# Performance work log

Measured on AMD Instinct MI355X. Metric: run time of the kernel, lower is better.

The kernel has to match this reference:

```python
import jax, jax.numpy as jnp
import numpy as np

E, K, CAP = 6, 2, 192
ALPHA, LOAD_PEN, MIN_USE, TEMP = 0.7, 2.0, 0.05, 1.0
BN_EPS = 1e-5
NEG = -1e30


def conv3x3(x, w, b=None):
    y = jax.lax.conv_general_dilated(x, w, (1, 1), 'SAME',
                                     dimension_numbers=('NCHW', 'OIHW', 'NCHW'))
    if b is not None:
        y = y + b[None, :, None, None]
    return y


def bn_eval(x, g, b):
    # fresh BatchNorm buffers: running_mean=0, running_var=1
    s = g / jnp.sqrt(1.0 + BN_EPS)
    return x * s[None, :, None, None] + b[None, :, None, None]


def maxpool2(x):
    return jax.lax.reduce_window(x, -jnp.inf, jax.lax.max,
                                 (1, 1, 2, 2), (1, 1, 2, 2), 'VALID')


def avgpool_to2(x):
    B, C, H, W = x.shape
    return x.reshape(B, C, 2, H // 2, 2, W // 2).mean(axis=(3, 5))


def expert_forward(p, x):
    h = jax.nn.relu(bn_eval(conv3x3(x, p['c1w'], p['c1b']), p['b1g'], p['b1b']))
    h = maxpool2(h)  # 32 -> 16
    h = jax.nn.relu(bn_eval(conv3x3(h, p['c2w'], p['c2b']), p['b2g'], p['b2b']))
    h = jax.nn.relu(bn_eval(conv3x3(h, p['c3w'], p['c3b']), p['b3g'], p['b3b']))
    h = maxpool2(h)  # 16 -> 8
    h = jax.nn.relu(bn_eval(conv3x3(h, p['c4w'], p['c4b']), p['b4g'], p['b4b']))
    h = jax.nn.relu(bn_eval(conv3x3(h, p['c5w'], p['c5b']), p['b5g'], p['b5b']))
    feat = h.mean(axis=(2, 3))                       # global avg pool -> [B, c3]
    f = jax.nn.relu(feat @ p['fw'].T + p['fb'])      # [B, feat_dim]
    return f @ p['cw'].T + p['cb']                   # [B, num_classes]


def moe_forward(x, t_c1w, t_b1g, t_b1b, t_c2w, t_b2g, t_b2b, t_fcw, t_fcb,
                g1w, g1b, g2w, g2b,
                e_c1w, e_c1b, e_b1g, e_b1b, e_c2w, e_c2b, e_b2g, e_b2b,
                e_c3w, e_c3b, e_b3g, e_b3b, e_c4w, e_c4b, e_b4g, e_b4b,
                e_c5w, e_c5b, e_b5g, e_b5b, e_fw, e_fb, e_cw, e_cb, ema):
    B = x.shape[0]
    # --- routing trunk ---
    h = jax.nn.relu(bn_eval(conv3x3(x, t_c1w), t_b1g, t_b1b))
    h = jax.nn.relu(bn_eval(conv3x3(h, t_c2w), t_b2g, t_b2b))
    h = avgpool_to2(maxpool2(h)).reshape(B, -1)      # [B, 128]
    rf = jax.nn.relu(h @ t_fcw.T + t_fcb)            # [B, routing_dim]
    # --- gate (eval: no dropout, no noise) ---
    g = jax.nn.relu(rf @ g1w.T + g1b)
    gate_scores = (g @ g2w.T + g2b) / TEMP           # [B, E]
    # --- all experts on full batch (dense, as in source) ---
    ep = {'c1w': e_c1w, 'c1b': e_c1b, 'b1g': e_b1g, 'b1b': e_b1b,
          'c2w': e_c2w, 'c2b': e_c2b, 'b2g': e_b2g, 'b2b': e_b2b,
          'c3w': e_c3w, 'c3b': e_c3b, 'b3g': e_b3g, 'b3b': e_b3b,
          'c4w': e_c4w, 'c4b': e_c4b, 'b4g': e_b4g, 'b4b': e_b4b,
          'c5w': e_c5w, 'c5b': e_c5b, 'b5g': e_b5g, 'b5b': e_b5b,
          'fw': e_fw, 'fb': e_fb, 'cw': e_cw, 'cb': e_cb}
    logits_e = jax.vmap(expert_forward, in_axes=(0, None))(ep, x)  # [E, B, C]
    logits_e = jnp.transpose(logits_e, (1, 0, 2))                   # [B, E, C]
    # confidence = -entropy = sum p*log(p)
    logp = jax.nn.log_softmax(logits_e, axis=2)
    conf = (jnp.exp(logp) * jnp.log(jnp.exp(logp) + 1e-12)).sum(axis=2)  # [B, E]
    # --- balanced scores ---
    combined = ALPHA * gate_scores + (1.0 - ALPHA) * conf
    boost = jnp.where(ema < MIN_USE, (MIN_USE - ema) * 10.0, 0.0)
    combined = combined + boost[None, :]
    balanced = combined - LOAD_PEN * ema[None, :]
    # --- greedy capacity-constrained dispatch (deterministic order, eval) ---
    _, topk_idx = jax.lax.top_k(balanced, K)          # [B, K]

    def step(loads, idxs):
        l = loads[idxs]                                # [K]
        fits = l < CAP
        first = jnp.argmax(fits)                       # first expert with room
        fallback = idxs[jnp.argmin(l)]
        chosen = jnp.where(fits.any(), idxs[first], fallback)
        return loads.at[chosen].add(1.0), chosen

    _, chosen = jax.lax.scan(step, jnp.zeros((E,), balanced.dtype), topk_idx)
    D = jax.nn.one_hot(chosen, E, dtype=bool)          # [B, E]
    # --- weighted combine ---
    masked = jnp.where(D, balanced, NEG)
    w = jax.nn.softmax(masked, axis=1) * D.astype(balanced.dtype)
    w = w / (w.sum(axis=1, keepdims=True) + 1e-12)
    logits_final = (w[:, :, None] * logits_e).sum(axis=1)  # [B, C]
    return logits_final, balanced, D


def _params(key):
    ks = iter(jax.random.split(key, 64))
    rd, rd2, fd, nc, c1, c2, c3 = 64, 32, 128, 10, 32, 64, 128

    def w(shape, fan):
        return jax.random.normal(next(ks), shape, jnp.float32) * np.sqrt(2.0 / fan)

    p = {}
    p['t_c1w'] = w((32, 3, 3, 3), 32 * 9); p['t_b1g'] = jnp.ones(32); p['t_b1b'] = jnp.zeros(32)
    p['t_c2w'] = w((32, 32, 3, 3), 32 * 9); p['t_b2g'] = jnp.ones(32); p['t_b2b'] = jnp.zeros(32)
    p['t_fcw'] = w((rd, 128), rd); p['t_fcb'] = jnp.zeros(rd)
    p['g1w'] = w((rd2, rd), rd2); p['g1b'] = jnp.zeros(rd2)
    p['g2w'] = w((E, rd2), E); p['g2b'] = jnp.zeros(E)
    for i, (ci, co) in enumerate([(3, c1), (c1, c2), (c2, c2), (c2, c3), (c3, c3)], 1):
        p[f'e_c{i}w'] = w((E, co, ci, 3, 3), co * 9)
        p[f'e_c{i}b'] = jnp.zeros((E, co))
        p[f'e_b{i}g'] = jnp.ones((E, co))
        p[f'e_b{i}b'] = jnp.zeros((E, co))
    p['e_fw'] = w((E, fd, c3), fd); p['e_fb'] = jnp.zeros((E, fd))
    p['e_cw'] = w((E, nc, fd), nc); p['e_cb'] = jnp.zeros((E, nc))
    p['ema'] = jnp.ones((E,), jnp.float32) / E
    return p


def setup_inputs() -> dict:
    key = jax.random.key(0)
    kx, kp = jax.random.split(key)
    inp = {'x': jax.random.normal(kx, (1024, 3, 32, 32), jnp.float32)}
    inp.update(_params(kp))
    return inp


def reference(x, t_c1w, t_b1g, t_b1b, t_c2w, t_b2g, t_b2b, t_fcw, t_fcb,
              g1w, g1b, g2w, g2b,
              e_c1w, e_c1b, e_b1g, e_b1b, e_c2w, e_c2b, e_b2g, e_b2b,
              e_c3w, e_c3b, e_b3g, e_b3b, e_c4w, e_c4b, e_b4g, e_b4b,
              e_c5w, e_c5b, e_b5g, e_b5b, e_fw, e_fb, e_cw, e_cb, ema):
    return moe_forward(x, t_c1w, t_b1g, t_b1b, t_c2w, t_b2g, t_b2b, t_fcw, t_fcb,
                       g1w, g1b, g2w, g2b,
                       e_c1w, e_c1b, e_b1g, e_b1b, e_c2w, e_c2b, e_b2g, e_b2b,
                       e_c3w, e_c3b, e_b3g, e_b3b, e_c4w, e_c4b, e_b4g, e_b4b,
                       e_c5w, e_c5b, e_b5g, e_b5b, e_fw, e_fb, e_cw, e_cb, ema)
```

## Files before the change

kernel.cpp:

```cpp
#include <hip/hip_runtime.h>
#include <math.h>

#define B_ 1024
#define E_ 6

typedef _Float16 half8 __attribute__((ext_vector_type(8)));
typedef float f32x4 __attribute__((ext_vector_type(4)));

__device__ __forceinline__ unsigned short h_bits(_Float16 h) {
    union { _Float16 f; unsigned short u; } c; c.f = h; return c.u;
}
__device__ __forceinline__ unsigned int splitpack(float v) {
    _Float16 h = (_Float16)v;
    _Float16 l = (_Float16)((v - (float)h) * 2048.0f);
    return (unsigned int)h_bits(h) | ((unsigned int)h_bits(l) << 16);
}

__global__ void prep_w(const float* __restrict__ w, const float* __restrict__ g,
                       float* __restrict__ wout, int CO, int CI, int total) {
    int i = blockIdx.x * 256 + threadIdx.x;
    if (i >= total) return;
    int k = i % 9;
    int t = i / 9;
    int ci = t % CI; t /= CI;
// ... 154 lines not shown
                }
                *(uint4*)(po + base + cobase + j4) = u;
            }
        }
    } else {
        float* out = (float*)outv;
        if constexpr (POOL) {
            constexpr int HP = H / 2;
            int py = ty / 2 + oy;
            int pxx = tx / 2 + ox;
#pragma unroll
            for (int g2 = 0; g2 < GPT; ++g2)
#pragma unroll
                for (int j = 0; j < CO_BLK; ++j) {
                    int co = (cg0s + g2 * G) * CO_BLK + j;
                    int a = g2 * CO_BLK + j;
                    float m = fmaxf(fmaxf(acc[0][a], acc[1][a]), fmaxf(acc[2][a], acc[3][a]));
                    out[((long)n * CO + co) * (HP * HP) + py * HP + pxx] = fmaxf(m, 0.0f);
                }
        } else {
            int yy = ty + oy;
            int xx = tx + ox;
#pragma unroll
            for (int g2 = 0; g2 < GPT; ++g2)
#pragma unroll
                for (int j = 0; j < CO_BLK; ++j) {
                    int co = (cg0s + g2 * G) * CO_BLK + j;
                    out[((long)n * CO + co) * (H * H) + yy * H + xx] =
                        fmaxf(acc[0][g2 * CO_BLK + j], 0.0f);
                }
        }
    }
}

__launch_bounds__(256, 2)
__global__ void conv_mfma_t2(const unsigned int* __restrict__ in,
                             const _Float16* __restrict__ wt,
                             const float* __restrict__ bias,
                             float* __restrict__ rf, int n0) {
    constexpr int PXS = 40;
    __shared__ _Float16 ldsH[18 * 18 * PXS];
    __shared__ _Float16 ldsL[18 * 18 * PXS];
    __shared__ float red[4][32];

    const int tid = threadIdx.x;
    const int wv = tid >> 6, lane = tid & 63;
    const int q = lane >> 4, l15 = lane & 15;
    const int bid = blockIdx.x;
    const int nl = bid >> 2, tile = bid & 3;
    const int ty2 = (tile >> 1) * 16, tx2 = (tile & 1) * 16;

    f32x4 accH[8], accL[8];
#pragma unroll
    for (int i = 0; i < 8; ++i) { accH[i] = (f32x4){0,0,0,0}; accL[i] = (f32x4){0,0,0,0}; }

    for (int u = tid; u < 18 * 18 * 8; u += 256) {
        int cu = u & 7;
        int p = u >> 3;
        int wy = p / 18, wx = p % 18;
        int gy = ty2 + wy - 1, gx = tx2 + wx - 1;
        uint4 w = make_uint4(0, 0, 0, 0);
        if ((unsigned)gy < 32u && (unsigned)gx < 32u)
            w = *(const uint4*)(in + ((long)nl * 1024 + gy * 32 + gx) * 32 + cu * 4);
        unsigned int h01 = (w.x & 0xffffu) | (w.y << 16);
        unsigned int h23 = (w.z & 0xffffu) | (w.w << 16);
        unsigned int l01 = (w.x >> 16) | (w.y & 0xffff0000u);
        unsigned int l23 = (w.z >> 16) | (w.w & 0xffff0000u);
        int fi = (wy * 18 + wx) * PXS + cu * 4;
        *(uint2*)(&ldsH[fi]) = make_uint2(h01, h23);
        *(uint2*)(&ldsL[fi]) = make_uint2(l01, l23);
    }
    __syncthreads();

#pragma unroll
    for (int ky = 0; ky < 3; ++ky)
#pragma unroll
        for (int kx = 0; kx < 3; ++kx) {
            const int tap = ky * 3 + kx;
            half8 ah[4], al[4];
#pragma unroll
            for (int mb = 0; mb < 4; ++mb) {
                int y = wv * 4 + mb;
                int fi = ((y + ky) * 18 + (l15 + kx)) * PXS + q * 8;
                ah[mb] = *(const half8*)&ldsH[fi];
                al[mb] = *(const half8*)&ldsL[fi];
            }
            half8 bh[2], bl[2];
#pragma unroll
            for (int nb = 0; nb < 2; ++nb) {
                int F0 = (nb * 9 + tap) * 2;
                bh[nb] = ((const half8*)wt)[(long)F0 * 64 + lane];
                bl[nb] = ((const half8*)wt)[(long)(F0 + 1) * 64 + lane];
            }
#pragma unroll
            for (int nb = 0; nb < 2; ++nb)
#pragma unroll
                for (int mb = 0; mb < 4; ++mb)
                    accH[mb * 2 + nb] = __builtin_amdgcn_mfma_f32_16x16x32_f16(
                        ah[mb], bh[nb], accH[mb * 2 + nb], 0, 0, 0);
#pragma unroll
            for (int nb = 0; nb < 2; ++nb)
#pragma unroll
                for (int mb = 0; mb < 4; ++mb)
                    accL[mb * 2 + nb] = __builtin_amdgcn_mfma_f32_16x16x32_f16(
                        ah[mb], bl[nb], accL[mb * 2 + nb], 0, 0, 0);
#pragma unroll
            for (int nb = 0; nb < 2; ++nb)
#pragma unroll
                for (int mb = 0; mb < 4; ++mb)
                    accL[mb * 2 + nb] = __builtin_amdgcn_mfma_f32_16x16x32_f16(
                        al[mb], bh[nb], accL[mb * 2 + nb], 0, 0, 0);
        }

    const float inv2048 = 1.0f / 2048.0f;
    float bv[2];
#pragma unroll
    for (int nb = 0; nb < 2; ++nb) bv[nb] = bias[nb * 16 + l15];
    float avg[2] = {0.0f, 0.0f};
#pragma unroll
    for (int k = 0; k < 2; ++k)
#pragma unroll
        for (int j = 0; j < 2; ++j)
#pragma unroll
            for (int nb = 0; nb < 2; ++nb) {
                float m = -1e30f;
#pragma unroll
                for (int dm = 0; dm < 2; ++dm)
#pragma unroll
                    for (int dr = 0; dr < 2; ++dr) {
                        int a = (2 * k + dm) * 2 + nb;
                        int r = 2 * j + dr;
                        float v = accH[a][r] + accL[a][r] * inv2048 + bv[nb];
                        m = fmaxf(m, v);
                    }
                avg[nb] += fmaxf(m, 0.0f);
            }
#pragma unroll
    for (int nb = 0; nb < 2; ++nb) {
        avg[nb] += __shfl_xor(avg[nb], 16);
        avg[nb] += __shfl_xor(avg[nb], 32);
    }
    if (q == 0) {
        red[wv][l15] = avg[0];
        red[wv][16 + l15] = avg[1];
    }
    __syncthreads();
    if (tid < 32) {
        float s = red[0][tid] + red[1][tid] + red[2][tid] + red[3][tid];
        int n = n0 + nl;
        rf[(long)n * 128 + tid * 4 + (tile >> 1) * 2 + (tile & 1)] = s * (1.0f / 64.0f);
    }
}

__launch_bounds__(512, 2)
__global__ void conv_expert(const float* __restrict__ x,
                            const float* __restrict__ w1b, const float* __restrict__ b1b_,
                            const _Float16* __restrict__ wt2b, const float* __restrict__ b2b_,
                            const _Float16* __restrict__ wt3b, const float* __restrict__ b3b_,
                            const _Float16* __restrict__ wt4b, const float* __restrict__ b4b_,
                            const _Float16* __restrict__ wt5b, const float* __restrict__ b5b_,
                            float* __restrict__ featb) {
    __shared__ _Float16 pool[77760];
    _Float16* c2H = pool;
    _Float16* c2L = pool + 12960;
    _Float16* BH  = pool;
    _Float16* BL  = pool + 8000;
    float* xs  = (float*)(pool + 25920);
    float* w1s = (float*)(pool + 25920 + 6936);
    float* b1s = (float*)(pool + 25920 + 6936 + 1728);
    _Float16* AH = pool + 25920;
    _Float16* AL = pool + 51840;
    _Float16* CH = pool + 25920;
    _Float16* CL = pool + 41920;

    const int tid = threadIdx.x;
    const int wv = tid >> 6, lane = tid & 63;
    const int q = lane >> 4, l15 = lane & 15;
    const int rg = wv >> 1, ch2 = wv & 1;
    const int e = blockIdx.x >> 10;
    const int n = blockIdx.x & 1023;
    const float inv2048 = 1.0f / 2048.0f;

    const float* w1 = w1b + e * 864;
    const float* b1 = b1b_ + e * 32;
    const _Float16* wt2 = wt2b + (size_t)e * 36864;
    const float* b2 = b2b_ + e * 64;
    const _Float16* wt3 = wt3b + (size_t)e * 73728;
    const float* b3 = b3b_ + e * 64;
    const _Float16* wt4 = wt4b + (size_t)e * 147456;
    const float* b4 = b4b_ + e * 128;
    const _Float16* wt5 = wt5b + (size_t)e * 294912;
    const float* b5 = b5b_ + e * 128;
    float* feat = featb + (size_t)e * (B_ * 128);

    {
        half8 z = {};
        half8* zp = (half8*)pool;
        for (int i = tid; i < 3240; i += 512) zp[i] = z;
    }
    for (int i = tid; i < 864; i += 512) w1s[i] = w1[i];
    if (tid < 32) b1s[tid] = b1[tid];
    for (int i = tid; i < 3 * 1156; i += 512) {
        int c = i / 1156;
        int r = i - c * 1156;
        int yy = r / 34 - 1, xx = r % 34 - 1;
        float v = 0.0f;
        if ((unsigned)yy < 32u && (unsigned)xx < 32u)
            v = x[((long)n * 3 + c) * 1024 + yy * 32 + xx];
        xs[i] = v;
    }
    __syncthreads();

    {
        const int pix = tid & 255;
        const int py1 = pix >> 4, px1 = pix & 15;
        const int coh = tid >> 8;
#pragma unroll
        for (int cg = 0; cg < 2; ++cg) {
            const int cog = coh * 2 + cg;
            float a[4][8];
#pragma unroll
            for (int j = 0; j < 8; ++j) {
                float bvv = b1s[cog * 8 + j];
#pragma unroll
                for (int p = 0; p < 4; ++p) a[p][j] = bvv;
            }
            for (int ci = 0; ci < 3; ++ci) {
                float patch[16];
#pragma unroll
                for (int r = 0; r < 4; ++r)
#pragma unroll
                    for (int cpx = 0; cpx < 4; ++cpx)
                        patch[r * 4 + cpx] = xs[ci * 1156 + (2 * py1 + r) * 34 + (2 * px1 + cpx)];
#pragma unroll
                for (int ky = 0; ky < 3; ++ky)
#pragma unroll
                    for (int kx = 0; kx < 3; ++kx) {
                        const float* wr = &w1s[((ci * 3 + ky) * 3 + kx) * 32 + cog * 8];
#pragma unroll
                        for (int j = 0; j < 8; ++j) {
                            float wvv = wr[j];
#pragma unroll
                            for (int dy = 0; dy < 2; ++dy)
#pragma unroll
                                for (int dx = 0; dx < 2; ++dx)
                                    a[dy * 2 + dx][j] =
                                        fmaf(patch[(dy + ky) * 4 + (dx + kx)], wvv,
                                             a[dy * 2 + dx][j]);
                        }
                    }
            }
            int fibase = ((py1 + 1) * 18 + (px1 + 1)) * 40 + cog * 8;
#pragma unroll
            for (int j = 0; j < 8; ++j) {
                float m = fmaxf(fmaxf(a[0][j], a[1][j]), fmaxf(a[2][j], a[3][j]));
                m = fmaxf(m, 0.0f);
                _Float16 hi = (_Float16)m;
                _Float16 lo = (_Float16)((m - (float)hi) * 2048.0f);
                c2H[fibase + j] = hi;
                c2L[fibase + j] = lo;
            }
        }
    }
    __syncthreads();

    for (int u = tid; u < 2 * 68 * 5; u += 512) {
        int g = u % 5;
        int t2 = u / 5;
        int ck = t2 / 68;
        int rp = t2 % 68;
        int wy, wx;
        if (rp < 18) { wy = 0; wx = rp; }
        else if (rp < 36) { wy = 17; wx = rp - 18; }
        else if (rp < 52) { wy = rp - 35; wx = 0; }
        else { wy = rp - 51; wx = 17; }
        int fi = ck * 12960 + (wy * 18 + wx) * 40 + g * 8;
        *(uint4*)(&AH[fi]) = make_uint4(0, 0, 0, 0);
        *(uint4*)(&AL[fi]) = make_uint4(0, 0, 0, 0);
    }

    f32x4 accH[8], accL[8];
#pragma unroll
    for (int i = 0; i < 8; ++i) { accH[i] = (f32x4){0,0,0,0}; accL[i] = (f32x4){0,0,0,0}; }

#pragma unroll
    for (int ky = 0; ky < 3; ++ky)
#pragma unroll
        for (int kx = 0; kx < 3; ++kx) {
            const int tap = ky * 3 + kx;
            half8 ah[4], al[4];
#pragma unroll
            for (int mb = 0; mb < 4; ++mb) {
                int y = rg * 4 + mb;
                int fi = ((y + ky) * 18 + (l15 + kx)) * 40 + q * 8;
                ah[mb] = *(const half8*)&c2H[fi];
                al[mb] = *(const half8*)&c2L[fi];
            }
            half8 bh[2], bl[2];
#pragma unroll
            for (int nb = 0; nb < 2; ++nb) {
                int nbg = ch2 * 2 + nb;
                int F0 = (nbg * 9 + tap) * 2;
                bh[nb] = ((const half8*)wt2)[(long)F0 * 64 + lane];
                bl[nb] = ((const half8*)wt2)[(long)(F0 + 1) * 64 + lane];
            }
#pragma unroll
            for (int nb = 0; nb < 2; ++nb)
#pragma unroll
                for (int mb = 0; mb < 4; ++mb)
                    accH[mb * 2 + nb] = __builtin_amdgcn_mfma_f32_16x16x32_f16(
                        ah[mb], bh[nb], accH[mb * 2 + nb], 0, 0, 0);
#pragma unroll
            for (int nb = 0; nb < 2; ++nb)
#pragma unroll
                for (int mb = 0; mb < 4; ++mb)
                    accL[mb * 2 + nb] = __builtin_amdgcn_mfma_f32_16x16x32_f16(
                        ah[mb], bl[nb], accL[mb * 2 + nb], 0, 0, 0);
#pragma unroll
            for (int nb = 0; nb < 2; ++nb)
#pragma unroll
                for (int mb = 0; mb < 4; ++mb)
                    accL[mb * 2 + nb] = __builtin_amdgcn_mfma_f32_16x16x32_f16(
                        al[mb], bh[nb], accL[mb * 2 + nb], 0, 0, 0);
        }
    {
        float bv[2];
#pragma unroll
        for (int nb = 0; nb < 2; ++nb) bv[nb] = b2[ch2 * 32 + nb * 16 + l15];
#pragma unroll
        for (int mb = 0; mb < 4; ++mb) {
            int y = rg * 4 + mb;
#pragma unroll
            for (int r = 0; r < 4; ++r) {
                int p = (y + 1) * 18 + (q * 4 + r + 1);
#pragma unroll
                for (int nb = 0; nb < 2; ++nb) {
                    float v = accH[mb * 2 + nb][r] + accL[mb * 2 + nb][r] * inv2048 + bv[nb];
                    v = fmaxf(v, 0.0f);
                    _Float16 hi = (_Float16)v;
                    _Float16 lo = (_Float16)((v - (float)hi) * 2048.0f);
                    int fi = ch2 * 12960 + p * 40 + nb * 16 + l15;
                    AH[fi] = hi;
                    AL[fi] = lo;
                }
            }
        }
    }
    __syncthreads();

#pragma unroll
    for (int i = 0; i < 8; ++i) { accH[i] = (f32x4){0,0,0,0}; accL[i] = (f32x4){0,0,0,0}; }

    for (int c = 0; c < 2; ++c) {
#pragma unroll
        for (int ky = 0; ky < 3; ++ky)
#pragma unroll
            for (int kx = 0; kx < 3; ++kx) {
                const int tap = ky * 3 + kx;
                half8 ah[4], al[4];
#pragma unroll
                for (int mb = 0; mb < 4; ++mb) {
                    int y = rg * 4 + mb;
                    int fi = c * 12960 + ((y + ky) * 18 + (l15 + kx)) * 40 + q * 8;
                    ah[mb] = *(const half8*)&AH[fi];
                    al[mb] = *(const half8*)&AL[fi];
                }
                half8 bh[2], bl[2];
#pragma unroll
                for (int nb = 0; nb < 2; ++nb) {
                    int nbg = ch2 * 2 + nb;
                    int F0 = ((nbg * 9 + tap) * 2 + c) * 2;
                    bh[nb] = ((const half8*)wt3)[(long)F0 * 64 + lane];
                    bl[nb] = ((const half8*)wt3)[(long)(F0 + 1) * 64 + lane];
                }
#pragma unroll
                for (int nb = 0; nb < 2; ++nb)
#pragma unroll
                    for (int mb = 0; mb < 4; ++mb)
                        accH[mb * 2 + nb] = __builtin_amdgcn_mfma_f32_16x16x32_f16(
                            ah[mb], bh[nb], accH[mb * 2 + nb], 0, 0, 0);
#pragma unroll
                for (int nb = 0; nb < 2; ++nb)
#pragma unroll
                    for (int mb = 0; mb < 4; ++mb)
                        accL[mb * 2 + nb] = __builtin_amdgcn_mfma_f32_16x16x32_f16(
                            ah[mb], bl[nb], accL[mb * 2 + nb], 0, 0, 0);
#pragma unroll
                for (int nb = 0; nb < 2; ++nb)
#pragma unroll
                    for (int mb = 0; mb < 4; ++mb)
                        accL[mb * 2 + nb] = __builtin_amdgcn_mfma_f32_16x16x32_f16(
                            al[mb], bh[nb], accL[mb * 2 + nb], 0, 0, 0);
            }
    }
    __syncthreads();

    for (int u = tid; u < 2 * 36 * 4; u += 512) {
        int g = u & 3;
        int t2 = u >> 2;
        int ck = t2 / 36;
        int rp = t2 % 36;
        int wy, wx;
        if (rp < 10) { wy = 0; wx = rp; }
        else if (rp < 20) { wy = 9; wx = rp - 10; }
        else if (rp < 28) { wy = rp - 19; wx = 0; }
        else { wy = rp - 27; wx = 9; }
        int fi = ck * 4000 + (wy * 10 + wx) * 40 + g * 8;
        *(uint4*)(&BH[fi]) = make_uint4(0, 0, 0, 0);
        *(uint4*)(&BL[fi]) = make_uint4(0, 0, 0, 0);
    }
    for (int u = tid; u < 4 * 36 * 4; u += 512) {
        int g = u & 3;
        int t2 = u >> 2;
        int ck = t2 / 36;
        int rp = t2 % 36;
        int wy, wx;
        if (rp < 10) { wy = 0; wx = rp; }
        else if (rp < 20) { wy = 9; wx = rp - 10; }
        else if (rp < 28) { wy = rp - 19; wx = 0; }
        else { wy = rp - 27; wx = 9; }
        int fi = ck * 4000 + (wy * 10 + wx) * 40 + g * 8;
        *(uint4*)(&CH[fi]) = make_uint4(0, 0, 0, 0);
        *(uint4*)(&CL[fi]) = make_uint4(0, 0, 0, 0);
    }
    {
        float bv[2];
#pragma unroll
        for (int nb = 0; nb < 2; ++nb) bv[nb] = b3[ch2 * 32 + nb * 16 + l15];
#pragma unroll
        for (int k = 0; k < 2; ++k)
#pragma unroll
            for (int j = 0; j < 2; ++j) {
                int yy = rg * 2 + k;
                int xx = q * 2 + j;
                int p = (yy + 1) * 10 + (xx + 1);
#pragma unroll
                for (int nb = 0; nb < 2; ++nb) {
                    float m = -1e30f;
#pragma unroll
                    for (int dm = 0; dm < 2; ++dm)
#pragma unroll
                        for (int dr = 0; dr < 2; ++dr) {
                            int a = (2 * k + dm) * 2 + nb;
                            int r = 2 * j + dr;
                            float v = accH[a][r] + accL[a][r] * inv2048 + bv[nb];
                            m = fmaxf(m, v);
                        }
                    m = fmaxf(m, 0.0f);
                    _Float16 hi = (_Float16)m;
                    _Float16 lo = (_Float16)((m - (float)hi) * 2048.0f);
                    int fi = ch2 * 4000 + p * 40 + nb * 16 + l15;
                    BH[fi] = hi;
                    BL[fi] = lo;
                }
            }
    }
    __syncthreads();

#pragma unroll
    for (int i = 0; i < 4; ++i) { accH[i] = (f32x4){0,0,0,0}; accL[i] = (f32x4){0,0,0,0}; }

    for (int c = 0; c < 2; ++c) {
#pragma unroll
        for (int ky = 0; ky < 3; ++ky)
#pragma unroll
            for (int kx = 0; kx < 3; ++kx) {
                const int tap = ky * 3 + kx;
                half8 ah[4], al[4];
#pragma unroll
                for (int mb = 0; mb < 4; ++mb) {
                    int m = mb * 16 + l15;
                    int p = ((m >> 3) + ky) * 10 + ((m & 7) + kx);
                    int fi = c * 4000 + p * 40 + q * 8;
                    ah[mb] = *(const half8*)&BH[fi];
                    al[mb] = *(const half8*)&BL[fi];
                }
                half8 bh, bl;
                {
                    int F0 = ((wv * 9 + tap) * 2 + c) * 2;
                    bh = ((const half8*)wt4)[(long)F0 * 64 + lane];
                    bl = ((const half8*)wt4)[(long)(F0 + 1) * 64 + lane];
                }
#pragma unroll
                for (int mb = 0; mb < 4; ++mb)
                    accH[mb] = __builtin_amdgcn_mfma_f32_16x16x32_f16(ah[mb], bh, accH[mb], 0, 0, 0);
#pragma unroll
                for (int mb = 0; mb < 4; ++mb)
                    accL[mb] = __builtin_amdgcn_mfma_f32_16x16x32_f16(ah[mb], bl, accL[mb], 0, 0, 0);
#pragma unroll
                for (int mb = 0; mb < 4; ++mb)
                    accL[mb] = __builtin_amdgcn_mfma_f32_16x16x32_f16(al[mb], bh, accL[mb], 0, 0, 0);
            }
    }
    {
        float bv = b4[wv * 16 + l15];
#pragma unroll
        for (int mb = 0; mb < 4; ++mb)
#pragma unroll
            for (int r = 0; r < 4; ++r) {
                int px = mb * 16 + q * 4 + r;
                int p = ((px >> 3) + 1) * 10 + ((px & 7) + 1);
                float v = accH[mb][r] + accL[mb][r] * inv2048 + bv;
                v = fmaxf(v, 0.0f);
                _Float16 hi = (_Float16)v;
                _Float16 lo = (_Float16)((v - (float)hi) * 2048.0f);
                int fi = (wv >> 1) * 4000 + p * 40 + (wv & 1) * 16 + l15;
                CH[fi] = hi;
                CL[fi] = lo;
            }
    }
    __syncthreads();

#pragma unroll
    for (int i = 0; i < 4; ++i) { accH[i] = (f32x4){0,0,0,0}; accL[i] = (f32x4){0,0,0,0}; }

    for (int c = 0; c < 4; ++c) {
#pragma unroll
        for (int ky = 0; ky < 3; ++ky)
#pragma unroll
            for (int kx = 0; kx < 3; ++kx) {
                const int tap = ky * 3 + kx;
                half8 ah[4], al[4];
#pragma unroll
                for (int mb = 0; mb < 4; ++mb) {
                    int m = mb * 16 + l15;
                    int p = ((m >> 3) + ky) * 10 + ((m & 7) + kx);
                    int fi = c * 4000 + p * 40 + q * 8;
                    ah[mb] = *(const half8*)&CH[fi];
                    al[mb] = *(const half8*)&CL[fi];
                }
                half8 bh, bl;
                {
                    int F0 = ((wv * 9 + tap) * 4 + c) * 2;
                    bh = ((const half8*)wt5)[(long)F0 * 64 + lane];
                    bl = ((const half8*)wt5)[(long)(F0 + 1) * 64 + lane];
                }
#pragma unroll
                for (int mb = 0; mb < 4; ++mb)
                    accH[mb] = __builtin_amdgcn_mfma_f32_16x16x32_f16(ah[mb], bh, accH[mb], 0, 0, 0);
#pragma unroll
                for (int mb = 0; mb < 4; ++mb)
                    accL[mb] = __builtin_amdgcn_mfma_f32_16x16x32_f16(ah[mb], bl, accL[mb], 0, 0, 0);
#pragma unroll
                for (int mb = 0; mb < 4; ++mb)
                    accL[mb] = __builtin_amdgcn_mfma_f32_16x16x32_f16(al[mb], bh, accL[mb], 0, 0, 0);
            }
    }
    {
        float bv = b5[wv * 16 + l15];
        float s = 0.0f;
#pragma unroll
        for (int mb = 0; mb < 4; ++mb)
#pragma unroll
            for (int r = 0; r < 4; ++r) {
                float v = accH[mb][r] + accL[mb][r] * inv2048 + bv;
                s += fmaxf(v, 0.0f);
            }
        s += __shfl_xor(s, 16);
        s += __shfl_xor(s, 32);
        if (lane < 16)
            feat[(long)n * 128 + wv * 16 + l15] = s * (1.0f / 64.0f);
    }
}

__launch_bounds__(128)
__global__ void head_k(const float* __restrict__ featb, const float* __restrict__ fwb,
                       const float* __restrict__ fbb, const float* __restrict__ cwb,
                       const float* __restrict__ cbb, float* __restrict__ outlb) {
    __shared__ float fe[128];
    __shared__ float fv[128];
    int e = blockIdx.x >> 10;
    int n = blockIdx.x & 1023;
    int t = threadIdx.x;
    const float* feat = featb + (size_t)e * (B_ * 128);
    const float* fw = fwb + (size_t)e * 16384;
    const float* fb = fbb + e * 128;
    const float* cw = cwb + (size_t)e * 1280;
    const float* cb = cbb + e * 10;
    float* outl = outlb + (size_t)e * (B_ * 10);

    fe[t] = feat[(long)n * 128 + t];
    __syncthreads();
    const float* wr = fw + t * 128;
    float a = fb[t];
#pragma unroll 8
    for (int k = 0; k < 128; ++k) a = fmaf(fe[k], wr[k], a);
    fv[t] = fmaxf(a, 0.0f);
    __syncthreads();
    if (t < 10) {
        const float* cr = cw + t * 128;
        float a2 = cb[t];
#pragma unroll 8
        for (int k = 0; k < 128; ++k) a2 = fmaf(fv[k], cr[k], a2);
        outl[n * 10 + t] = a2;
    }
}

template <int I, int O, bool RELU>
__global__ void fc_k(const float* __restrict__ in, const float* __restrict__ W,
                     const float* __restrict__ bias, float* __restrict__ out) {
    int g = blockIdx.x * 256 + threadIdx.x;
    if (g >= B_ * O) return;
    int n = g / O;
    int o = g - n * O;
    const float* ip = in + (long)n * I;
    const float* wp = W + (long)o * I;
    float a = bias[o];
#pragma unroll 8
    for (int k = 0; k < I; ++k) a = fmaf(ip[k], wp[k], a);
    if (RELU) a = fmaxf(a, 0.0f);
    out[g] = a;
}

__global__ void conf_bal_k(const float* __restrict__ logitsE, const float* __restrict__ gate,
                           const float* __restrict__ ema, float* __restrict__ balanced,
                           unsigned char* __restrict__ cand) {
    int b = blockIdx.x * 256 + threadIdx.x;
    if (b >= B_) return;
    float bal[E_];
#pragma unroll
    for (int e = 0; e < E_; ++e) {
        const float* lp = logitsE + ((long)e * B_ + b) * 10;
        float m = lp[0];
#pragma unroll
        for (int k = 1; k < 10; ++k) m = fmaxf(m, lp[k]);
        float s = 0.0f;
#pragma unroll
        for (int k = 0; k < 10; ++k) s += expf(lp[k] - m);
        float ls = m + logf(s);
        float conf = 0.0f;
#pragma unroll
        for (int k = 0; k < 10; ++k) {
            float pp = expf(lp[k] - ls);
            conf += pp * logf(pp + 1e-12f);
        }
        float em = ema[e];
        float boost = (em < 0.05f) ? (0.05f - em) * 10.0f : 0.0f;
        bal[e] = 0.7f * gate[b * E_ + e] + 0.3f * conf + boost - 2.0f * em;
        balanced[b * E_ + e] = bal[e];
    }
    int i0 = 0;
    float m0 = bal[0];
#pragma unroll
    for (int e = 1; e < E_; ++e)
        if (bal[e] > m0) { m0 = bal[e]; i0 = e; }
    int i1 = -1;
    float m1 = -1e38f;
#pragma unroll
    for (int e = 0; e < E_; ++e)
        if (e != i0 && bal[e] > m1) { m1 = bal[e]; i1 = e; }
    cand[b] = (unsigned char)(i0 | (i1 << 3));
}

__global__ void dispatch_k(const unsigned char* __restrict__ cand, int* __restrict__ chosen) {
    int lane = threadIdx.x;
    unsigned long long L = 0;
    for (int r = 0; r < 16; ++r) {
        unsigned int v = cand[r * 64 + lane];
        int ch = 0;
        for (int q2 = 0; q2 < 64; ++q2) {
            unsigned int s = (unsigned int)__builtin_amdgcn_readlane((int)v, q2);
            unsigned int i0 = s & 7u;
            unsigned int i1 = (s >> 3) & 7u;
            unsigned int a0 = (unsigned int)(L >> (i0 * 10)) & 1023u;
            unsigned int a1 = (unsigned int)(L >> (i1 * 10)) & 1023u;
            unsigned int fb = (a1 < a0) ? i1 : i0;
            unsigned int c = (a0 < 192u) ? i0 : ((a1 < 192u) ? i1 : fb);
            if (lane == q2) ch = (int)c;
            L += 1ull << (c * 10);
        }
        chosen[r * 64 + lane] = ch;
    }
}

__global__ void final_k(const float* __restrict__ logitsE, const int* __restrict__ chosen,
                        float* __restrict__ out) {
    int b = blockIdx.x * 256 + threadIdx.x;
    if (b >= B_) return;
    int c = chosen[b];
    const float w = 1.0f / (1.0f + 1e-12f);
    const float* lp = logitsE + ((long)c * B_ + b) * 10;
#pragma unroll
    for (int k = 0; k < 10; ++k) out[b * 10 + k] = lp[k] * w;
    float* Dp = out + B_ * 10 + B_ * E_ + b * E_;
#pragma unroll
    for (int e = 0; e < E_; ++e) Dp[e] = (e == c) ? 1.0f : 0.0f;
}

extern "C" void kernel_launch(void* const* d_in, const int* in_sizes, int n_in,
                              void* d_out, int out_size, void* d_ws, size_t ws_size,
                              hipStream_t stream) {
    (void)in_sizes; (void)n_in; (void)out_size; (void)ws_size;
    const float* x     = (const float*)d_in[0];
    const float* t_c1w = (const float*)d_in[1];
    const float* t_b1g = (const float*)d_in[2];
    const float* t_b1b = (const float*)d_in[3];
    const float* t_c2w = (const float*)d_in[4];
    const float* t_b2g = (const float*)d_in[5];
    const float* t_b2b = (const float*)d_in[6];
    const float* t_fcw = (const float*)d_in[7];
    const float* t_fcb = (const float*)d_in[8];
    const float* g1w   = (const float*)d_in[9];
    const float* g1b   = (const float*)d_in[10];
    const float* g2w   = (const float*)d_in[11];
    const float* g2b   = (const float*)d_in[12];
    const float* e_c1w = (const float*)d_in[13];
    const float* e_c1b = (const float*)d_in[14];
    const float* e_b1g = (const float*)d_in[15];
    const float* e_b1b = (const float*)d_in[16];
    const float* e_c2w = (const float*)d_in[17];
    const float* e_c2b = (const float*)d_in[18];
    const float* e_b2g = (const float*)d_in[19];
    const float* e_b2b = (const float*)d_in[20];
    const float* e_c3w = (const float*)d_in[21];
    const float* e_c3b = (const float*)d_in[22];
    const float* e_b3g = (const float*)d_in[23];
    const float* e_b3b = (const float*)d_in[24];
    const float* e_c4w = (const float*)d_in[25];
    const float* e_c4b = (const float*)d_in[26];
    const float* e_b4g = (const float*)d_in[27];
    const float* e_b4b = (const float*)d_in[28];
    const float* e_c5w = (const float*)d_in[29];
    const float* e_c5b = (const float*)d_in[30];
    const float* e_b5g = (const float*)d_in[31];
    const float* e_b5b = (const float*)d_in[32];
    const float* e_fw  = (const float*)d_in[33];
    const float* e_fb  = (const float*)d_in[34];
    const float* e_cw  = (const float*)d_in[35];
    const float* e_cb  = (const float*)d_in[36];
    const float* ema   = (const float*)d_in[37];
    float* out = (float*)d_out;
    float* ws  = (float*)d_ws;

    size_t o = 0;
    float* R1f = ws + o; o += 8388608;
    float* R2f = ws + o; o += 16777216;
    float* rf_in   = ws + o; o += B_ * 128;
    float* rf      = ws + o; o += B_ * 64;
    float* gv      = ws + o; o += B_ * 32;
    float* gate    = ws + o; o += B_ * E_;
    float* logitsE = ws + o; o += E_ * B_ * 10;
    float* featb   = ws + o; o += (size_t)E_ * B_ * 128;
    int*   chosen  = (int*)(ws + o); o += B_;
    unsigned char* cand = (unsigned char*)(ws + o); o += 256;
    float* wt_t1 = ws + o; o += 864;
    float* bt_t1 = ws + o; o += 32;
    float* bt_t2 = ws + o; o += 32;
    float* wt_c1 = ws + o; o += 6 * 864;
    float* bt_c1 = ws + o; o += 6 * 32;
    float* bt_c2 = ws + o; o += 6 * 64;
    float* bt_c3 = ws + o; o += 6 * 64;
    float* bt_c4 = ws + o; o += 6 * 128;
    float* bt_c5 = ws + o; o += 6 * 128;
    _Float16* wfrag_t2 = (_Float16*)(ws + o); o += 9216;
    _Float16* wfrag_c2 = (_Float16*)(ws + o); o += 110592;
    _Float16* wfrag_c3 = (_Float16*)(ws + o); o += 221184;
    _Float16* wfrag_c4 = (_Float16*)(ws + o); o += 442368;
    _Float16* wfrag_c5 = (_Float16*)(ws + o); o += 884736;

    unsigned int* R2u = (unsigned int*)R2f;
    (void)R1f;

    auto gsz = [](int n) { return (n + 255) / 256; };
    prep_w<<<gsz(864), 256, 0, stream>>>(t_c1w, t_b1g, wt_t1, 32, 3, 864);
    prep_b<<<1, 256, 0, stream>>>(nullptr, t_b1g, t_b1b, bt_t1, 32);
    prep_wfrag<<<gsz(9216), 256, 0, stream>>>(t_c2w, t_b2g, wfrag_t2, 32, 32, 9216);
    prep_b<<<1, 256, 0, stream>>>(nullptr, t_b2g, t_b2b, bt_t2, 32);
    prep_w<<<gsz(5184), 256, 0, stream>>>(e_c1w, e_b1g, wt_c1, 32, 3, 5184);
    prep_b<<<1, 256, 0, stream>>>(e_c1b, e_b1g, e_b1b, bt_c1, 192);
    prep_wfrag<<<gsz(110592), 256, 0, stream>>>(e_c2w, e_b2g, wfrag_c2, 32, 64, 110592);
    prep_b<<<2, 256, 0, stream>>>(e_c2b, e_b2g, e_b2b, bt_c2, 384);
    prep_wfrag<<<gsz(221184), 256, 0, stream>>>(e_c3w, e_b3g, wfrag_c3, 64, 64, 221184);
    prep_b<<<2, 256, 0, stream>>>(e_c3b, e_b3g, e_b3b, bt_c3, 384);
    prep_wfrag<<<gsz(442368), 256, 0, stream>>>(e_c4w, e_b4g, wfrag_c4, 64, 128, 442368);
    prep_b<<<3, 256, 0, stream>>>(e_c4b, e_b4g, e_b4b, bt_c4, 768);
    prep_wfrag<<<gsz(884736), 256, 0, stream>>>(e_c5w, e_b5g, wfrag_c5, 128, 128, 884736);
    prep_b<<<3, 256, 0, stream>>>(e_c5b, e_b5g, e_b5b, bt_c5, 768);

    for (int q = 0; q < 2; ++q) {
        const float* xq = x + (size_t)q * 512 * 3 * 1024;
        conv3x3<3, 32, 32, 16, 32, 3, false, 1><<<512 * 4, 256, 0, stream>>>(
            xq, wt_t1, bt_t1, (void*)R2u);
        conv_mfma_t2<<<512 * 4, 256, 0, stream>>>(R2u, wfrag_t2, bt_t2, rf_in, q * 512);
    }
    fc_k<128, 64, true><<<256, 256, 0, stream>>>(rf_in, t_fcw, t_fcb, rf);
    fc_k<64, 32, true><<<128, 256, 0, stream>>>(rf, g1w, g1b, gv);
    fc_k<32, 6, false><<<24, 256, 0, stream>>>(gv, g2w, g2b, gate);

    conv_expert<<<E_ * B_, 512, 0, stream>>>(
        x, wt_c1, bt_c1, wfrag_c2, bt_c2, wfrag_c3, bt_c3,
        wfrag_c4, bt_c4, wfrag_c5, bt_c5, featb);
    head_k<<<E_ * B_, 128, 0, stream>>>(featb, e_fw, e_fb, e_cw, e_cb, logitsE);

    float* balanced = out + B_ * 10;
    conf_bal_k<<<4, 256, 0, stream>>>(logitsE, gate, ema, balanced, cand);
    dispatch_k<<<1, 64, 0, stream>>>(cand, chosen);
    final_k<<<4, 256, 0, stream>>>(logitsE, chosen, out);
}
```

Before: 1.325 ms.

## Double conv_expert block to 1024 threads, splitting MFMA tiles across 16 waves

Expands the fused per-image expert conv kernel from 8 to 16 waves. Each wave now handles half the output rows or pixels in every conv stage, with smaller accumulator and fragment arrays. Conv4/5 add a pixel-half split and a shared-memory reduction for the global average pool. The aim is more latency hiding per block, since LDS use (~155KB) already limits occupancy to one block per CU. The cost is duplicated weight-fragment loads per wave and an extra barrier.

```diff
diff --git a/kernel.cpp b/kernel.cpp
--- a/kernel.cpp
+++ b/kernel.cpp
@@ -330,7 +330,7 @@
     }
 }
 
-__launch_bounds__(512, 2)
+__launch_bounds__(1024, 1)
 __global__ void conv_expert(const float* __restrict__ x,
                             const float* __restrict__ w1b, const float* __restrict__ b1b_,
                             const _Float16* __restrict__ wt2b, const float* __restrict__ b2b_,
@@ -354,7 +354,8 @@
     const int tid = threadIdx.x;
     const int wv = tid >> 6, lane = tid & 63;
     const int q = lane >> 4, l15 = lane & 15;
-    const int rg = wv >> 1, ch2 = wv & 1;
+    const int rg3 = wv >> 1, ch2 = wv & 1;
+    const int nbg45 = wv >> 1, ph45 = wv & 1;
     const int e = blockIdx.x >> 10;
     const int n = blockIdx.x & 1023;
     const float inv2048 = 1.0f / 2048.0f;
@@ -374,11 +375,11 @@
     {
         half8 z = {};
         half8* zp = (half8*)pool;
-        for (int i = tid; i < 3240; i += 512) zp[i] = z;
-    }
-    for (int i = tid; i < 864; i += 512) w1s[i] = w1[i];
-    if (tid < 32) b1s[tid] = b1[tid];
-    for (int i = tid; i < 3 * 1156; i += 512) {
+        for (int i = tid; i < 3240; i += 1024) zp[i] = z;
+    }
+    if (tid < 864) w1s[tid] = w1[tid];
+    if (tid >= 896 && tid < 928) b1s[tid - 896] = b1[tid - 896];
+    for (int i = tid; i < 3 * 1156; i += 1024) {
         int c = i / 1156;
         int r = i - c * 1156;
         int yy = r / 34 - 1, xx = r % 34 - 1;
@@ -392,57 +393,53 @@
     {
         const int pix = tid & 255;
         const int py1 = pix >> 4, px1 = pix & 15;
-        const int coh = tid >> 8;
-#pragma unroll
-        for (int cg = 0; cg < 2; ++cg) {
-            const int cog = coh * 2 + cg;
-            float a[4][8];
-#pragma unroll
-            for (int j = 0; j < 8; ++j) {
-                float bvv = b1s[cog * 8 + j];
-#pragma unroll
-                for (int p = 0; p < 4; ++p) a[p][j] = bvv;
-            }
-            for (int ci = 0; ci < 3; ++ci) {
-                float patch[16];
-#pragma unroll
-                for (int r = 0; r < 4; ++r)
-#pragma unroll
-                    for (int cpx = 0; cpx < 4; ++cpx)
-                        patch[r * 4 + cpx] = xs[ci * 1156 + (2 * py1 + r) * 34 + (2 * px1 + cpx)];
-#pragma unroll
-                for (int ky = 0; ky < 3; ++ky)
-#pragma unroll
-                    for (int kx = 0; kx < 3; ++kx) {
-                        const float* wr = &w1s[((ci * 3 + ky) * 3 + kx) * 32 + cog * 8];
-#pragma unroll
-                        for (int j = 0; j < 8; ++j) {
-                            float wvv = wr[j];
-#pragma unroll
-                            for (int dy = 0; dy < 2; ++dy)
-#pragma unroll
-                                for (int dx = 0; dx < 2; ++dx)
-                                    a[dy * 2 + dx][j] =
-                                        fmaf(patch[(dy + ky) * 4 + (dx + kx)], wvv,
-                                             a[dy * 2 + dx][j]);
-                        }
+        const int cog = tid >> 8;
+        float a[4][8];
+#pragma unroll
+        for (int j = 0; j < 8; ++j) {
+            float bvv = b1s[cog * 8 + j];
+#pragma unroll
+            for (int p = 0; p < 4; ++p) a[p][j] = bvv;
+        }
+        for (int ci = 0; ci < 3; ++ci) {
+            float patch[16];
+#pragma unroll
+            for (int r = 0; r < 4; ++r)
+#pragma unroll
+                for (int cpx = 0; cpx < 4; ++cpx)
+                    patch[r * 4 + cpx] = xs[ci * 1156 + (2 * py1 + r) * 34 + (2 * px1 + cpx)];
+#pragma unroll
+            for (int ky = 0; ky < 3; ++ky)
+#pragma unroll
+                for (int kx = 0; kx < 3; ++kx) {
+                    const float* wr = &w1s[((ci * 3 + ky) * 3 + kx) * 32 + cog * 8];
+#pragma unroll
+                    for (int j = 0; j < 8; ++j) {
+                        float wvv = wr[j];
+#pragma unroll
+                        for (int dy = 0; dy < 2; ++dy)
+#pragma unroll
+                            for (int dx = 0; dx < 2; ++dx)
+                                a[dy * 2 + dx][j] =
+                                    fmaf(patch[(dy + ky) * 4 + (dx + kx)], wvv,
+                                         a[dy * 2 + dx][j]);
                     }
-            }
-            int fibase = ((py1 + 1) * 18 + (px1 + 1)) * 40 + cog * 8;
-#pragma unroll
-            for (int j = 0; j < 8; ++j) {
-                float m = fmaxf(fmaxf(a[0][j], a[1][j]), fmaxf(a[2][j], a[3][j]));
-                m = fmaxf(m, 0.0f);
-                _Float16 hi = (_Float16)m;
-                _Float16 lo = (_Float16)((m - (float)hi) * 2048.0f);
-                c2H[fibase + j] = hi;
-                c2L[fibase + j] = lo;
-            }
+                }
+        }
+        int fibase = ((py1 + 1) * 18 + (px1 + 1)) * 40 + cog * 8;
+#pragma unroll
+        for (int j = 0; j < 8; ++j) {
+            float m = fmaxf(fmaxf(a[0][j], a[1][j]), fmaxf(a[2][j], a[3][j]));
+            m = fmaxf(m, 0.0f);
+            _Float16 hi = (_Float16)m;
+            _Float16 lo = (_Float16)((m - (float)hi) * 2048.0f);
+            c2H[fibase + j] = hi;
+            c2L[fibase + j] = lo;
         }
     }
     __syncthreads();
 
-    for (int u = tid; u < 2 * 68 * 5; u += 512) {
+    for (int u = tid; u < 2 * 68 * 5; u += 1024) {
         int g = u % 5;
         int t2 = u / 5;
         int ck = t2 / 68;
@@ -457,19 +454,19 @@
         *(uint4*)(&AL[fi]) = make_uint4(0, 0, 0, 0);
     }
 
-    f32x4 accH[8], accL[8];
-#pragma unroll
-    for (int i = 0; i < 8; ++i) { accH[i] = (f32x4){0,0,0,0}; accL[i] = (f32x4){0,0,0,0}; }
+    f32x4 accH[4], accL[4];
+#pragma unroll
+    for (int i = 0; i < 4; ++i) { accH[i] = (f32x4){0,0,0,0}; accL[i] = (f32x4){0,0,0,0}; }
 
 #pragma unroll
     for (int ky = 0; ky < 3; ++ky)
 #pragma unroll
         for (int kx = 0; kx < 3; ++kx) {
             const int tap = ky * 3 + kx;
-            half8 ah[4], al[4];
-#pragma unroll
-            for (int mb = 0; mb < 4; ++mb) {
-                int y = rg * 4 + mb;
+            half8 ah[2], al[2];
+#pragma unroll
+            for (int mb = 0; mb < 2; ++mb) {
+                int y = rg3 * 2 + mb;
                 int fi = ((y + ky) * 18 + (l15 + kx)) * 40 + q * 8;
                 ah[mb] = *(const half8*)&c2H[fi];
                 al[mb] = *(const half8*)&c2L[fi];
@@ -485,19 +482,19 @@
 #pragma unroll
             for (int nb = 0; nb < 2; ++nb)
 #pragma unroll
-                for (int mb = 0; mb < 4; ++mb)
+                for (int mb = 0; mb < 2; ++mb)
                     accH[mb * 2 + nb] = __builtin_amdgcn_mfma_f32_16x16x32_f16(
                         ah[mb], bh[nb], accH[mb * 2 + nb], 0, 0, 0);
 #pragma unroll
             for (int nb = 0; nb < 2; ++nb)
 #pragma unroll
-                for (int mb = 0; mb < 4; ++mb)
+                for (int mb = 0; mb < 2; ++mb)
                     accL[mb * 2 + nb] = __builtin_amdgcn_mfma_f32_16x16x32_f16(
                         ah[mb], bl[nb], accL[mb * 2 + nb], 0, 0, 0);
 #pragma unroll
             for (int nb = 0; nb < 2; ++nb)
 #pragma unroll
-                for (int mb = 0; mb < 4; ++mb)
+                for (int mb = 0; mb < 2; ++mb)
                     accL[mb * 2 + nb] = __builtin_amdgcn_mfma_f32_16x16x32_f16(
                         al[mb], bh[nb], accL[mb * 2 + nb], 0, 0, 0);
         }
@@ -506,8 +503,8 @@
 #pragma unroll
         for (int nb = 0; nb < 2; ++nb) bv[nb] = b2[ch2 * 32 + nb * 16 + l15];
 #pragma unroll
-        for (int mb = 0; mb < 4; ++mb) {
-            int y = rg * 4 + mb;
+        for (int mb = 0; mb < 2; ++mb) {
+            int y = rg3 * 2 + mb;
 #pragma unroll
             for (int r = 0; r < 4; ++r) {
                 int p = (y + 1) * 18 + (q * 4 + r + 1);
@@ -527,7 +524,7 @@
     __syncthreads();
 
 #pragma unroll
-    for (int i = 0; i < 8; ++i) { accH[i] = (f32x4){0,0,0,0}; accL[i] = (f32x4){0,0,0,0}; }
+    for (int i = 0; i < 4; ++i) { accH[i] = (f32x4){0,0,0,0}; accL[i] = (f32x4){0,0,0,0}; }
 
     for (int c = 0; c < 2; ++c) {
 #pragma unroll
@@ -535,10 +532,10 @@
 #pragma unroll
             for (int kx = 0; kx < 3; ++kx) {
                 const int tap = ky * 3 + kx;
-                half8 ah[4], al[4];
-#pragma unroll
-                for (int mb = 0; mb < 4; ++mb) {
-                    int y = rg * 4 + mb;
+                half8 ah[2], al[2];
+#pragma unroll
+                for (int mb = 0; mb < 2; ++mb) {
+                    int y = rg3 * 2 + mb;
                     int fi = c * 12960 + ((y + ky) * 18 + (l15 + kx)) * 40 + q * 8;
                     ah[mb] = *(const half8*)&AH[fi];
                     al[mb] = *(const half8*)&AL[fi];
@@ -554,26 +551,26 @@
 #pragma unroll
                 for (int nb = 0; nb < 2; ++nb)
 #pragma unroll
-                    for (int mb = 0; mb < 4; ++mb)
+                    for (int mb = 0; mb < 2; ++mb)
                         accH[mb * 2 + nb] = __builtin_amdgcn_mfma_f32_16x16x32_f16(
                             ah[mb], bh[nb], accH[mb * 2 + nb], 0, 0, 0);
 #pragma unroll
                 for (int nb = 0; nb < 2; ++nb)
 #pragma unroll
-                    for (int mb = 0; mb < 4; ++mb)
+                    for (int mb = 0; mb < 2; ++mb)
                         accL[mb * 2 + nb] = __builtin_amdgcn_mfma_f32_16x16x32_f16(
                             ah[mb], bl[nb], accL[mb * 2 + nb], 0, 0, 0);
 #pragma unroll
                 for (int nb = 0; nb < 2; ++nb)
 #pragma unroll
-                    for (int mb = 0; mb < 4; ++mb)
+                    for (int mb = 0; mb < 2; ++mb)
                         accL[mb * 2 + nb] = __builtin_amdgcn_mfma_f32_16x16x32_f16(
                             al[mb], bh[nb], accL[mb * 2 + nb], 0, 0, 0);
             }
     }
     __syncthreads();
 
-    for (int u = tid; u < 2 * 36 * 4; u += 512) {
+    for (int u = tid; u < 2 * 36 * 4; u += 1024) {
         int g = u & 3;
         int t2 = u >> 2;
         int ck = t2 / 36;
@@ -587,7 +584,7 @@
         *(uint4*)(&BH[fi]) = make_uint4(0, 0, 0, 0);
         *(uint4*)(&BL[fi]) = make_uint4(0, 0, 0, 0);
     }
-    for (int u = tid; u < 4 * 36 * 4; u += 512) {
+    for (int u = tid; u < 4 * 36 * 4; u += 1024) {
         int g = u & 3;
         int t2 = u >> 2;
         int ck = t2 / 36;
@@ -606,37 +603,34 @@
 #pragma unroll
         for (int nb = 0; nb < 2; ++nb) bv[nb] = b3[ch2 * 32 + nb * 16 + l15];
 #pragma unroll
-        for (int k = 0; k < 2; ++k)
-#pragma unroll
-            for (int j = 0; j < 2; ++j) {
-                int yy = rg * 2 + k;
-                int xx = q * 2 + j;
-                int p = (yy + 1) * 10 + (xx + 1);
-#pragma unroll
-                for (int nb = 0; nb < 2; ++nb) {
-                    float m = -1e30f;
-#pragma unroll
-                    for (int dm = 0; dm < 2; ++dm)
-#pragma unroll
-                        for (int dr = 0; dr < 2; ++dr) {
-                            int a = (2 * k + dm) * 2 + nb;
-                            int r = 2 * j + dr;
-                            float v = accH[a][r] + accL[a][r] * inv2048 + bv[nb];
-                            m = fmaxf(m, v);
-                        }
-                    m = fmaxf(m, 0.0f);
-                    _Float16 hi = (_Float16)m;
-                    _Float16 lo = (_Float16)((m - (float)hi) * 2048.0f);
-                    int fi = ch2 * 4000 + p * 40 + nb * 16 + l15;
-                    BH[fi] = hi;
-                    BL[fi] = lo;
-                }
-            }
+        for (int j = 0; j < 2; ++j) {
+            int xx = q * 2 + j;
+            int p = (rg3 + 1) * 10 + (xx + 1);
+#pragma unroll
+            for (int nb = 0; nb < 2; ++nb) {
+                float m = -1e30f;
+#pragma unroll
+                for (int dm = 0; dm < 2; ++dm)
+#pragma unroll
+                    for (int dr = 0; dr < 2; ++dr) {
+                        int a = dm * 2 + nb;
+                        int r = 2 * j + dr;
+                        float v = accH[a][r] + accL[a][r] * inv2048 + bv[nb];
+                        m = fmaxf(m, v);
+                    }
+                m = fmaxf(m, 0.0f);
+                _Float16 hi = (_Float16)m;
+                _Float16 lo = (_Float16)((m - (float)hi) * 2048.0f);
+                int fi = ch2 * 4000 + p * 40 + nb * 16 + l15;
+                BH[fi] = hi;
+                BL[fi] = lo;
+            }
+        }
     }
     __syncthreads();
 
 #pragma unroll
-    for (int i = 0; i < 4; ++i) { accH[i] = (f32x4){0,0,0,0}; accL[i] = (f32x4){0,0,0,0}; }
+    for (int i = 0; i < 2; ++i) { accH[i] = (f32x4){0,0,0,0}; accL[i] = (f32x4){0,0,0,0}; }
 
     for (int c = 0; c < 2; ++c) {
 #pragma unroll
@@ -644,10 +638,10 @@
 #pragma unroll
             for (int kx = 0; kx < 3; ++kx) {
                 const int tap = ky * 3 + kx;
-                half8 ah[4], al[4];
-#pragma unroll
-                for (int mb = 0; mb < 4; ++mb) {
-                    int m = mb * 16 + l15;
+                half8 ah[2], al[2];
+#pragma unroll
+                for (int mb = 0; mb < 2; ++mb) {
+                    int m = ph45 * 32 + mb * 16 + l15;
                     int p = ((m >> 3) + ky) * 10 + ((m & 7) + kx);
                     int fi = c * 4000 + p * 40 + q * 8;
                     ah[mb] = *(const half8*)&BH[fi];
@@ -655,34 +649,34 @@
                 }
                 half8 bh, bl;
                 {
-                    int F0 = ((wv * 9 + tap) * 2 + c) * 2;
+                    int F0 = ((nbg45 * 9 + tap) * 2 + c) * 2;
                     bh = ((const half8*)wt4)[(long)F0 * 64 + lane];
                     bl = ((const half8*)wt4)[(long)(F0 + 1) * 64 + lane];
                 }
 #pragma unroll
-                for (int mb = 0; mb < 4; ++mb)
+                for (int mb = 0; mb < 2; ++mb)
                     accH[mb] = __builtin_amdgcn_mfma_f32_16x16x32_f16(ah[mb], bh, accH[mb], 0, 0, 0);
 #pragma unroll
-                for (int mb = 0; mb < 4; ++mb)
+                for (int mb = 0; mb < 2; ++mb)
                     accL[mb] = __builtin_amdgcn_mfma_f32_16x16x32_f16(ah[mb], bl, accL[mb], 0, 0, 0);
 #pragma unroll
-                for (int mb = 0; mb < 4; ++mb)
+                for (int mb = 0; mb < 2; ++mb)
                     accL[mb] = __builtin_amdgcn_mfma_f32_16x16x32_f16(al[mb], bh, accL[mb], 0, 0, 0);
             }
     }
     {
-        float bv = b4[wv * 16 + l15];
-#pragma unroll
-        for (int mb = 0; mb < 4; ++mb)
+        float bv = b4[nbg45 * 16 + l15];
+#pragma unroll
+        for (int mb = 0; mb < 2; ++mb)
 #pragma unroll
             for (int r = 0; r < 4; ++r) {
-                int px = mb * 16 + q * 4 + r;
+                int px = ph45 * 32 + mb * 16 + q * 4 + r;
                 int p = ((px >> 3) + 1) * 10 + ((px & 7) + 1);
                 float v = accH[mb][r] + accL[mb][r] * inv2048 + bv;
                 v = fmaxf(v, 0.0f);
                 _Float16 hi = (_Float16)v;
                 _Float16 lo = (_Float16)((v - (float)hi) * 2048.0f);
-                int fi = (wv >> 1) * 4000 + p * 40 + (wv & 1) * 16 + l15;
+                int fi = (nbg45 >> 1) * 4000 + p * 40 + (nbg45 & 1) * 16 + l15;
                 CH[fi] = hi;
                 CL[fi] = lo;
             }
@@ -690,7 +684,7 @@
     __syncthreads();
 
 #pragma unroll
-    for (int i = 0; i < 4; ++i) { accH[i] = (f32x4){0,0,0,0}; accL[i] = (f32x4){0,0,0,0}; }
+    for (int i = 0; i < 2; ++i) { accH[i] = (f32x4){0,0,0,0}; accL[i] = (f32x4){0,0,0,0}; }
 
     for (int c = 0; c < 4; ++c) {
 #pragma unroll
@@ -698,10 +692,10 @@
 #pragma unroll
             for (int kx = 0; kx < 3; ++kx) {
                 const int tap = ky * 3 + kx;
-                half8 ah[4], al[4];
-#pragma unroll
-                for (int mb = 0; mb < 4; ++mb) {
-                    int m = mb * 16 + l15;
+                half8 ah[2], al[2];
+#pragma unroll
+                for (int mb = 0; mb < 2; ++mb) {
+                    int m = ph45 * 32 + mb * 16 + l15;
                     int p = ((m >> 3) + ky) * 10 + ((m & 7) + kx);
                     int fi = c * 4000 + p * 40 + q * 8;
                     ah[mb] = *(const half8*)&CH[fi];
@@ -709,26 +703,26 @@
                 }
                 half8 bh, bl;
                 {
-                    int F0 = ((wv * 9 + tap) * 4 + c) * 2;
+                    int F0 = ((nbg45 * 9 + tap) * 4 + c) * 2;
                     bh = ((const half8*)wt5)[(long)F0 * 64 + lane];
                     bl = ((const half8*)wt5)[(long)(F0 + 1) * 64 + lane];
                 }
 #pragma unroll
-                for (int mb = 0; mb < 4; ++mb)
+                for (int mb = 0; mb < 2; ++mb)
                     accH[mb] = __builtin_amdgcn_mfma_f32_16x16x32_f16(ah[mb], bh, accH[mb], 0, 0, 0);
 #pragma unroll
-                for (int mb = 0; mb < 4; ++mb)
+                for (int mb = 0; mb < 2; ++mb)
                     accL[mb] = __builtin_amdgcn_mfma_f32_16x16x32_f16(ah[mb], bl, accL[mb], 0, 0, 0);
 #pragma unroll
-                for (int mb = 0; mb < 4; ++mb)
+                for (int mb = 0; mb < 2; ++mb)
                     accL[mb] = __builtin_amdgcn_mfma_f32_16x16x32_f16(al[mb], bh, accL[mb], 0, 0, 0);
             }
     }
     {
-        float bv = b5[wv * 16 + l15];
+        float bv = b5[nbg45 * 16 + l15];
         float s = 0.0f;
 #pragma unroll
-        for (int mb = 0; mb < 4; ++mb)
+        for (int mb = 0; mb < 2; ++mb)
 #pragma unroll
             for (int r = 0; r < 4; ++r) {
                 float v = accH[mb][r] + accL[mb][r] * inv2048 + bv;
@@ -736,8 +730,14 @@
             }
         s += __shfl_xor(s, 16);
         s += __shfl_xor(s, 32);
-        if (lane < 16)
-            feat[(long)n * 128 + wv * 16 + l15] = s * (1.0f / 64.0f);
+        float* red = (float*)pool;
+        if (lane < 16) red[wv * 16 + l15] = s;
+        __syncthreads();
+        if (tid < 128) {
+            int g = tid >> 4, l = tid & 15;
+            float t = red[(g * 2) * 16 + l] + red[(g * 2 + 1) * 16 + l];
+            feat[(long)n * 128 + g * 16 + l] = t * (1.0f / 64.0f);
+        }
     }
 }
 
@@ -965,7 +965,7 @@
     fc_k<64, 32, true><<<128, 256, 0, stream>>>(rf, g1w, g1b, gv);
     fc_k<32, 6, false><<<24, 256, 0, stream>>>(gv, g2w, g2b, gate);
 
-    conv_expert<<<E_ * B_, 512, 0, stream>>>(
+    conv_expert<<<E_ * B_, 1024, 0, stream>>>(
         x, wt_c1, bt_c1, wfrag_c2, bt_c2, wfrag_c3, bt_c3,
         wfrag_c4, bt_c4, wfrag_c5, bt_c5, featb);
     head_k<<<E_ * B_, 128, 0, stream>>>(featb, e_fw, e_fb, e_cw, e_cb, logitsE);
```

Measured after the change: 1.410 ms. +6.4%, slower.
